# Optimization experiments

Hardware: AMD Instinct MI355X
Metric: run time of the kernel (lower is better)

The kernel has to match this reference:

```python
import jax, jax.numpy as jnp
import numpy as np

WS = 14          # window size (SAM ViT default)
NUM_HEADS = 12   # dim=768 -> head_dim=64
THETA = 10000.0  # rope theta


def _axial_rope_cos_sin(head_dim, end_x, end_y):
    # compute_axial_cis: head_dim//4 freqs per axis; t_x = t % end_x, t_y = t // end_x
    n = head_dim // 4
    freqs = 1.0 / (THETA ** (np.arange(0, head_dim, 4)[:n].astype(np.float32) / head_dim))
    t = np.arange(end_x * end_y, dtype=np.float32)
    t_x = t % end_x
    t_y = np.floor(t / end_x)
    ang = np.concatenate([t_x[:, None] * freqs[None, :], t_y[:, None] * freqs[None, :]], axis=-1)
    return jnp.asarray(np.cos(ang)), jnp.asarray(np.sin(ang))  # (N, head_dim//2) each


def _apply_rope(x, cos, sin):
    # x: (B, N, D) viewed as complex pairs along last dim (torch.view_as_complex ordering)
    x2 = x.reshape(x.shape[:-1] + (-1, 2))
    xr, xi = x2[..., 0], x2[..., 1]
    out_r = xr * cos - xi * sin
    out_i = xr * sin + xi * cos
    return jnp.stack([out_r, out_i], axis=-1).reshape(x.shape)


def setup_inputs() -> dict:
    key = jax.random.key(0)
    ks = jax.random.split(key, 6)
    B, H, W, C = 8, 64, 64, 768
    hd = C // NUM_HEADS
    max_rel = 2 * WS - 1
    return {
        "x": jax.random.normal(ks[0], (B, H, W, C), dtype=jnp.float32),
        "qkv_w": jax.random.normal(ks[1], (3 * C, C), dtype=jnp.float32) * 0.02,
        "qkv_b": jnp.zeros((3 * C,), dtype=jnp.float32),
        "proj_w": jax.random.normal(ks[2], (C, C), dtype=jnp.float32) * 0.02,
        "proj_b": jnp.zeros((C,), dtype=jnp.float32),
        "rel_pos_h": jax.random.normal(ks[3], (max_rel, hd), dtype=jnp.float32) * 0.02,
        "rel_pos_w": jax.random.normal(ks[4], (max_rel, hd), dtype=jnp.float32) * 0.02,
    }


def reference(x, qkv_w, qkv_b, proj_w, proj_b, rel_pos_h, rel_pos_w):
    B, H, W, C = x.shape
    nH = NUM_HEADS
    hd = C // nH
    N = WS * WS

    # --- window_partition with padding ---
    pad_h = (-H) % WS
    pad_w = (-W) % WS
    xp = jnp.pad(x, ((0, 0), (0, pad_h), (0, pad_w), (0, 0)))
    Hp, Wp = H + pad_h, W + pad_w
    nwh, nww = Hp // WS, Wp // WS
    xw = xp.reshape(B, nwh, WS, nww, WS, C).transpose(0, 1, 3, 2, 4, 5).reshape(-1, N, C)
    Bw = xw.shape[0]  # B * num_windows

    # --- qkv projection, split heads ---
    qkv = xw @ qkv_w.T + qkv_b                       # (Bw, N, 3C)
    qkv = qkv.reshape(Bw, N, 3, nH, hd).transpose(2, 0, 3, 1, 4).reshape(3, Bw * nH, N, hd)
    q, k, v = qkv[0], qkv[1], qkv[2]

    # --- 2D axial rotary encoding on q, k ---
    cos, sin = _axial_rope_cos_sin(hd, WS, WS)       # (N, hd//2)
    q = _apply_rope(q, cos, sin)
    k = _apply_rope(k, cos, sin)

    # --- decomposed relative-position bias (get_rel_pos gather + einsum) ---
    coords = jnp.arange(WS)[:, None] - jnp.arange(WS)[None, :] + (WS - 1)  # (WS, WS) in [0, 2WS-2]
    Rh = rel_pos_h[coords]                           # (WS, WS, hd)
    Rw = rel_pos_w[coords]
    r_q = q.reshape(-1, WS, WS, hd)
    rel_h = jnp.einsum('bhwc,hkc->bhwk', r_q, Rh)    # (BwnH, WS, WS, WS)
    rel_w = jnp.einsum('bhwc,wkc->bhwk', r_q, Rw)

    # --- attention: q k^T / sqrt(hd) + rel biases (math of concat_rel_pos + sdpa) ---
    attn = jnp.einsum('bqc,bkc->bqk', q, k) * (hd ** -0.5)
    attn = attn.reshape(-1, WS, WS, WS, WS) + rel_h[..., :, None] + rel_w[..., None, :]
    attn = jax.nn.softmax(attn.reshape(-1, N, N), axis=-1)
    out = attn @ v                                   # (BwnH, N, hd)

    # --- merge heads, output projection ---
    out = out.reshape(Bw, nH, WS, WS, hd).transpose(0, 2, 3, 1, 4).reshape(Bw, N, C)
    out = out @ proj_w.T + proj_b

    # --- window_unpartition, crop padding ---
    out = out.reshape(B, nwh, nww, WS, WS, C).transpose(0, 1, 3, 2, 4, 5).reshape(B, Hp, Wp, C)
    return out[:, :H, :W, :]
```

## Files before the change

### kernel.cpp

```cpp
#include <hip/hip_runtime.h>

using u16 = unsigned short;
using u32 = unsigned int;

typedef __bf16 bf16x8 __attribute__((ext_vector_type(8)));
typedef float f32x4 __attribute__((ext_vector_type(4)));

#define M32 32768

__device__ __forceinline__ u16 f2bf(float f) {
  u32 u = __float_as_uint(f);
  u += 0x7fffu + ((u >> 16) & 1u);
  return (u16)(u >> 16);
}
__device__ __forceinline__ u32 pkbf(float a, float b) {
  return (u32)f2bf(a) | ((u32)f2bf(b) << 16);
}
__device__ __forceinline__ u32 cvtpk(float a, float b) {
  u32 r; asm("v_cvt_pk_bf16_f32 %0, %1, %2" : "=v"(r) : "v"(a), "v"(b)); return r;
}
__device__ __forceinline__ float bflo(u32 w) { return __uint_as_float(w << 16); }
__device__ __forceinline__ float bfhi(u32 w) { return __uint_as_float(w & 0xffff0000u); }

__device__ __forceinline__ void async16(const void* g, void* l) {
  __builtin_amdgcn_global_load_lds((const __attribute__((address_space(1))) void*)g,
                                   (__attribute__((address_space(3))) void*)l, 16, 0, 0);
}

union frag { uint4 u; bf16x8 b; };

__global__ __launch_bounds__(256) void prep_w(const float* __restrict__ qw,
                                              const float* __restrict__ pw,
                                              u16* __restrict__ qwb, u16* __restrict__ pwb,
                                              float2* __restrict__ cs) {
  int i = blockIdx.x * 256 + threadIdx.x;
  if (i < 2304 * 768) qwb[i] = f2bf(qw[i]);
  if (i < 768 * 768)  pwb[i] = f2bf(pw[i]);
  if (i < 196 * 32) {
    int t = i >> 5, f = i & 31;
    float fr = powf(10000.f, -(float)(f & 15) * (1.f / 16.f));
    float ang = (f < 16 ? (float)(t % 14) : (float)(t / 14)) * fr;
    cs[i] = make_float2(cosf(ang), sinf(ang));
  }
}

template<int EPI>
__global__ __launch_bounds__(256) void gemm_bt(
    const void* __restrict__ Av, const u16* __restrict__ B,
    const float* __restrict__ bias, u16* __restrict__ Cb,
    float* __restrict__ Cf, int K, int N, int NTI)
{
  __shared__ u16 As[128 * 32];
  __shared__ u16 Bs[128 * 32];

  const int nwg = gridDim.x;
  const int orig = blockIdx.x;
  const int q = nwg >> 3, r = nwg & 7;
  const int xcd = orig & 7, loc = orig >> 3;
  const int wg = (xcd < r ? xcd * (q + 1) : r * (q + 1) + (xcd - r) * q) + loc;
  const int m0 = (wg / NTI) * 128;
  const int n0 = (wg % NTI) * 128;

  const int tid = threadIdx.x;
  const int lane = tid & 63;
  const int wv = tid >> 6;
  const int wm = wv >> 1, wn = wv & 1;
  const int lr = lane & 15, lq = lane >> 4;

  f32x4 acc[4][4];
#pragma unroll
  for (int i = 0; i < 4; i++)
#pragma unroll
    for (int j = 0; j < 4; j++)
      acc[i][j] = f32x4{0.f, 0.f, 0.f, 0.f};

  const int srow = tid >> 2, sg = (tid & 3) * 8;
  const float* Af0 = (const float*)Av + (size_t)(m0 + srow) * K + sg;
  const u16*   Ab0 = (const u16*)Av + (size_t)(m0 + srow) * K + sg;
  const u16*   B0  = B + (size_t)(n0 + srow) * K + sg;

  for (int k0 = 0; k0 < K; k0 += 32) {
    __syncthreads();
    async16(B0 + k0, (void*)(Bs + tid * 8));
    async16(B0 + (size_t)64 * K + k0, (void*)(Bs + 2048 + tid * 8));
    if constexpr (EPI == 0) {
      float4 a0 = *(const float4*)(Af0 + k0);
      float4 a1 = *(const float4*)(Af0 + k0 + 4);
      float4 a2 = *(const float4*)(Af0 + (size_t)64 * K + k0);
      float4 a3 = *(const float4*)(Af0 + (size_t)64 * K + k0 + 4);
      *(uint4*)(As + tid * 8) =
          make_uint4(cvtpk(a0.x, a0.y), cvtpk(a0.z, a0.w), cvtpk(a1.x, a1.y), cvtpk(a1.z, a1.w));
      *(uint4*)(As + 2048 + tid * 8) =
          make_uint4(cvtpk(a2.x, a2.y), cvtpk(a2.z, a2.w), cvtpk(a3.x, a3.y), cvtpk(a3.z, a3.w));
    } else {
      async16(Ab0 + k0, (void*)(As + tid * 8));
      async16(Ab0 + (size_t)64 * K + k0, (void*)(As + 2048 + tid * 8));
    }
    __syncthreads();

    frag af[4], bg[4];
#pragma unroll
    for (int i = 0; i < 4; i++) {
      af[i].u = *(const uint4*)(As + (wm * 64 + i * 16 + lr) * 32 + lq * 8);
      bg[i].u = *(const uint4*)(Bs + (wn * 64 + i * 16 + lr) * 32 + lq * 8);
    }
#pragma unroll
    for (int i = 0; i < 4; i++)
#pragma unroll
      for (int j = 0; j < 4; j++)
        acc[i][j] = __builtin_amdgcn_mfma_f32_16x16x32_bf16(af[i].b, bg[j].b, acc[i][j], 0, 0, 0);
  }

#pragma unroll
  for (int i = 0; i < 4; i++) {
#pragma unroll
    for (int j = 0; j < 4; j++) {
      const int n = n0 + wn * 64 + j * 16 + lr;
      const int mb = m0 + wm * 64 + i * 16 + lq * 4;
      const float bv = bias[n];
#pragma unroll
      for (int rr = 0; rr < 4; rr++) {
        float val = acc[i][j][rr] + bv;
        int m = mb + rr;
        if (EPI == 0) Cb[(size_t)m * N + n] = f2bf(val);
        else          Cf[(size_t)m * N + n] = val;
      }
    }
  }
}

#define R1P 104
#define VTP 232
#define PQP 40
#define LDS_R1   (224 * R1P * 2)
#define LDS_VT   (64 * VTP * 2)
#define LDS_PB   (4 * 16 * PQP * 2)
#define LDS_TOT  (LDS_R1 + LDS_VT + LDS_PB)

__global__ __launch_bounds__(256, 2) void attn_mfma(
    const u16* __restrict__ qkv, u16* __restrict__ ao,
    const float* __restrict__ relph, const float* __restrict__ relpw,
    const float2* __restrict__ cs, const float* __restrict__ qb)
{
  extern __shared__ char smem[];
  u16*   R1  = (u16*)smem;
  u16*   VTb = (u16*)(smem + LDS_R1);
  u16*   Th  = VTb;
  u16*   Tw  = VTb + 256 * 28;
  char*  PBr = smem + LDS_R1 + LDS_VT;

  const int blk = blockIdx.x;
  const int w = blk / 12, h = blk % 12;
  const int tid = threadIdx.x;
  const int lane = tid & 63, wv = tid >> 6;
  const int lr = lane & 15, lq = lane >> 4;

  const int b0 = w / 25, rw_ = w % 25;
  const int wy = (rw_ / 5) * 14, wx = (rw_ % 5) * 14;
  const int ty = tid / 14, tx = tid - ty * 14;
  const int gh = wy + ty, gw = wx + tx;
  const bool inb = (tid < 196) && (gh < 64) && (gw < 64);
  const size_t grow = (size_t)((b0 * 64 + gh) * 64 + gw);

  {
    float qf[64];
    if (tid < 196) {
      if (inb) {
        const u16* qp = qkv + grow * 2304 + h * 64;
        uint4 q4[8];
#pragma unroll
        for (int u = 0; u < 8; u++) q4[u] = *(const uint4*)(qp + u * 8);
#pragma unroll
        for (int u = 0; u < 8; u++) {
          qf[u*8+0] = bflo(q4[u].x); qf[u*8+1] = bfhi(q4[u].x);
          qf[u*8+2] = bflo(q4[u].y); qf[u*8+3] = bfhi(q4[u].y);
          qf[u*8+4] = bflo(q4[u].z); qf[u*8+5] = bfhi(q4[u].z);
          qf[u*8+6] = bflo(q4[u].w); qf[u*8+7] = bfhi(q4[u].w);
        }
      } else {
        const float4* bp = (const float4*)(qb + h * 64);
#pragma unroll
        for (int u = 0; u < 16; u++) {
          float4 t4 = bp[u];
          qf[u*4+0] = t4.x; qf[u*4+1] = t4.y; qf[u*4+2] = t4.z; qf[u*4+3] = t4.w;
        }
      }
      const float2* ct = cs + tid * 32;
#pragma unroll
      for (int f = 0; f < 32; f++) {
        float2 c2 = ct[f];
        float xr = qf[2*f], xi = qf[2*f+1];
        qf[2*f]   = (xr * c2.x - xi * c2.y) * 0.125f;
        qf[2*f+1] = (xr * c2.y + xi * c2.x) * 0.125f;
      }
    } else {
#pragma unroll
      for (int d = 0; d < 64; d++) qf[d] = 0.f;
    }
    if (tid < 224) {
      u16* dst = R1 + tid * R1P;
#pragma unroll
      for (int u = 0; u < 8; u++)
        *(uint4*)(dst + u * 8) = make_uint4(pkbf(qf[u*8+0], qf[u*8+1]), pkbf(qf[u*8+2], qf[u*8+3]),
                                            pkbf(qf[u*8+4], qf[u*8+5]), pkbf(qf[u*8+6], qf[u*8+7]));
    }
  }
  __syncthreads();

  frag af[4][3];
#pragma unroll
  for (int i = 0; i < 4; i++)
#pragma unroll
    for (int kc = 0; kc < 2; kc++) {
      if (wv == 3 && i >= 2)
        af[i][kc].u = make_uint4(0u, 0u, 0u, 0u);
      else
        af[i][kc].u = *(const uint4*)(R1 + (wv * 64 + i * 16 + lr) * R1P + kc * 32 + lq * 8);
    }

#pragma unroll
  for (int n = 0; n < 2; n++) {
    f32x4 tah[4], taw[4];
#pragma unroll
    for (int i = 0; i < 4; i++) { tah[i] = f32x4{0,0,0,0}; taw[i] = f32x4{0,0,0,0}; }
    const int j = n * 16 + lr;
#pragma unroll
    for (int kc = 0; kc < 2; kc++) {
      float4 ha = {0,0,0,0}, hb = {0,0,0,0}, wa = {0,0,0,0}, wb2 = {0,0,0,0};
      if (j < 27) {
        const float* ph  = relph + j * 64 + kc * 32 + lq * 8;
        const float* pw2 = relpw + j * 64 + kc * 32 + lq * 8;
        ha = *(const float4*)ph;  hb  = *(const float4*)(ph + 4);
        wa = *(const float4*)pw2; wb2 = *(const float4*)(pw2 + 4);
      }
      frag bh, bw;
      bh.u = make_uint4(pkbf(ha.x, ha.y), pkbf(ha.z, ha.w), pkbf(hb.x, hb.y), pkbf(hb.z, hb.w));
      bw.u = make_uint4(pkbf(wa.x, wa.y), pkbf(wa.z, wa.w), pkbf(wb2.x, wb2.y), pkbf(wb2.z, wb2.w));
#pragma unroll
      for (int i = 0; i < 4; i++) {
        tah[i] = __builtin_amdgcn_mfma_f32_16x16x32_bf16(af[i][kc].b, bh.b, tah[i], 0, 0, 0);
        taw[i] = __builtin_amdgcn_mfma_f32_16x16x32_bf16(af[i][kc].b, bw.b, taw[i], 0, 0, 0);
      }
    }
    int jcol = n * 16 + lr;
    if (jcol < 28) {
#pragma unroll
      for (int i = 0; i < 4; i++)
#pragma unroll
        for (int r2 = 0; r2 < 4; r2++) {
          int qq = wv * 64 + i * 16 + lq * 4 + r2;
          Th[qq * 28 + jcol] = f2bf(tah[i][r2] * 8.f);
          Tw[qq * 28 + jcol] = f2bf(taw[i][r2] * 8.f);
        }
    }
  }
  __syncthreads();

  {
    u32 wb[16];
#pragma unroll
    for (int z = 0; z < 16; z++) wb[z] = 0;
    if (tid < 196) {
      const u16* thr = Th + tid * 28 + ty + 13;
      const u16* twr = Tw + tid * 28 + tx + 13;
#pragma unroll
      for (int p = 0; p < 7; p++) wb[p]     = (u32)thr[-(2*p)] | ((u32)thr[-(2*p+1)] << 16);
#pragma unroll
      for (int p = 0; p < 7; p++) wb[7 + p] = (u32)twr[-(2*p)] | ((u32)twr[-(2*p+1)] << 16);
    }
    wb[14] = 0xC1F0u;
    if (tid < 224) {
      u16* dst = R1 + tid * R1P + 64;
#pragma unroll
      for (int u = 0; u < 4; u++)
        *(uint4*)(dst + u * 8) = make_uint4(wb[u*4], wb[u*4+1], wb[u*4+2], wb[u*4+3]);
    }
  }
  __syncthreads();

#pragma unroll
  for (int i = 0; i < 4; i++) {
    if (wv == 3 && i >= 2)
      af[i][2].u = make_uint4(0u, 0u, 0u, 0u);
    else
      af[i][2].u = *(const uint4*)(R1 + (wv * 64 + i * 16 + lr) * R1P + 64 + lq * 8);
  }
  __syncthreads();

  if (tid < 224) {
    const bool real = tid < 196;
    u32 kw[32];
#pragma unroll
    for (int z = 0; z < 32; z++) kw[z] = 0;
    if (real) {
      float kf[64];
      if (inb) {
        const u16* kp = qkv + grow * 2304 + 768 + h * 64;
        uint4 k4[8];
#pragma unroll
        for (int u = 0; u < 8; u++) k4[u] = *(const uint4*)(kp + u * 8);
#pragma unroll
        for (int u = 0; u < 8; u++) {
          kf[u*8+0] = bflo(k4[u].x); kf[u*8+1] = bfhi(k4[u].x);
          kf[u*8+2] = bflo(k4[u].y); kf[u*8+3] = bfhi(k4[u].y);
          kf[u*8+4] = bflo(k4[u].z); kf[u*8+5] = bfhi(k4[u].z);
          kf[u*8+6] = bflo(k4[u].w); kf[u*8+7] = bfhi(k4[u].w);
        }
      } else {
        const float4* bp = (const float4*)(qb + 768 + h * 64);
#pragma unroll
        for (int u = 0; u < 16; u++) {
          float4 t4 = bp[u];
          kf[u*4+0] = t4.x; kf[u*4+1] = t4.y; kf[u*4+2] = t4.z; kf[u*4+3] = t4.w;
        }
      }
      const float2* ct = cs + tid * 32;
#pragma unroll
      for (int f = 0; f < 32; f++) {
        float2 c2 = ct[f];
        float xr = kf[2*f], xi = kf[2*f+1];
        kf[2*f]   = xr * c2.x - xi * c2.y;
        kf[2*f+1] = xr * c2.y + xi * c2.x;
      }
#pragma unroll
      for (int p = 0; p < 32; p++) kw[p] = pkbf(kf[2*p], kf[2*p+1]);
    }
    const int tA = real ? 64 + ty : 92;
    const int tB = real ? 78 + tx : 92;
    u32 aw[16];
#pragma unroll
    for (int p = 0; p < 16; p++) {
      const int c0 = 64 + 2 * p, c1 = c0 + 1;
      u32 lo = (c0 == tA || c0 == tB) ? 0x3F80u : 0u;
      u32 hi = (c1 == tA || c1 == tB) ? 0x3F80u : 0u;
      aw[p] = lo | (hi << 16);
    }
    u16* dst = R1 + tid * R1P;
#pragma unroll
    for (int u = 0; u < 8; u++)
      *(uint4*)(dst + u * 8) = make_uint4(kw[u*4], kw[u*4+1], kw[u*4+2], kw[u*4+3]);
#pragma unroll
    for (int u = 0; u < 4; u++)
      *(uint4*)(dst + 64 + u * 8) = make_uint4(aw[u*4], aw[u*4+1], aw[u*4+2], aw[u*4+3]);

    if (real) {
      u16* col = VTb + tid;
      if (inb) {
        const u16* vp = qkv + grow * 2304 + 1536 + h * 64;
#pragma unroll
        for (int u = 0; u < 8; u++) {
          uint4 v4 = *(const uint4*)(vp + u * 8);
          col[(u*8+0) * VTP] = (u16)(v4.x & 0xffff); col[(u*8+1) * VTP] = (u16)(v4.x >> 16);
          col[(u*8+2) * VTP] = (u16)(v4.y & 0xffff); col[(u*8+3) * VTP] = (u16)(v4.y >> 16);
          col[(u*8+4) * VTP] = (u16)(v4.z & 0xffff); col[(u*8+5) * VTP] = (u16)(v4.z >> 16);
          col[(u*8+6) * VTP] = (u16)(v4.w & 0xffff); col[(u*8+7) * VTP] = (u16)(v4.w >> 16);
        }
      } else {
        const float4* bp = (const float4*)(qb + 1536 + h * 64);
#pragma unroll
        for (int u = 0; u < 16; u++) {
          float4 t4 = bp[u];
          col[(u*4+0) * VTP] = f2bf(t4.x); col[(u*4+1) * VTP] = f2bf(t4.y);
          col[(u*4+2) * VTP] = f2bf(t4.z); col[(u*4+3) * VTP] = f2bf(t4.w);
        }
      }
    } else {
#pragma unroll
      for (int d = 0; d < 64; d++) VTb[d * VTP + tid] = 0;
    }
  }
  __syncthreads();

  f32x4 oacc[4][4];
  f32x4 lacc[4];
#pragma unroll
  for (int i = 0; i < 4; i++) {
    lacc[i] = f32x4{0,0,0,0};
#pragma unroll
    for (int j = 0; j < 4; j++) oacc[i][j] = f32x4{0,0,0,0};
  }
  frag ones;
  ones.u = make_uint4(0x3F803F80u, 0x3F803F80u, 0x3F803F80u, 0x3F803F80u);
  u16* PB = (u16*)PBr + wv * 16 * PQP;

  for (int c = 0; c < 7; c++) {
    frag bk[2][3];
#pragma unroll
    for (int kt = 0; kt < 2; kt++)
#pragma unroll
      for (int kc = 0; kc < 3; kc++)
        bk[kt][kc].u = *(const uint4*)(R1 + (c * 32 + kt * 16 + lr) * R1P + kc * 32 + lq * 8);

    frag bv[4];
#pragma unroll
    for (int j = 0; j < 4; j++)
      bv[j].u = *(const uint4*)(VTb + (j * 16 + lr) * VTP + c * 32 + lq * 8);

    f32x4 sacc[4][2];
#pragma unroll
    for (int i = 0; i < 4; i++) { sacc[i][0] = f32x4{0,0,0,0}; sacc[i][1] = f32x4{0,0,0,0}; }
#pragma unroll
    for (int kc = 0; kc < 3; kc++)
#pragma unroll
      for (int i = 0; i < 4; i++)
#pragma unroll
        for (int kt = 0; kt < 2; kt++)
          sacc[i][kt] = __builtin_amdgcn_mfma_f32_16x16x32_bf16(af[i][kc].b, bk[kt][kc].b, sacc[i][kt], 0, 0, 0);

#pragma unroll
    for (int i = 0; i < 4; i++) {
#pragma unroll
      for (int kt = 0; kt < 2; kt++)
#pragma unroll
        for (int r2 = 0; r2 < 4; r2++)
          PB[(lq * 4 + r2) * PQP + kt * 16 + lr] = f2bf(__expf(sacc[i][kt][r2]));

      frag pf;
      pf.u = *(const uint4*)(PB + lr * PQP + lq * 8);

      lacc[i] = __builtin_amdgcn_mfma_f32_16x16x32_bf16(pf.b, ones.b, lacc[i], 0, 0, 0);
#pragma unroll
      for (int j = 0; j < 4; j++)
        oacc[i][j] = __builtin_amdgcn_mfma_f32_16x16x32_bf16(pf.b, bv[j].b, oacc[i][j], 0, 0, 0);
    }
  }

#pragma unroll
  for (int i = 0; i < 4; i++) {
    f32x4 inv;
#pragma unroll
    for (int r2 = 0; r2 < 4; r2++) inv[r2] = 1.f / lacc[i][r2];
#pragma unroll
    for (int r2 = 0; r2 < 4; r2++) {
      int qq = wv * 64 + i * 16 + lq * 4 + r2;
      if (qq < 196) {
        int qy = qq / 14, qx = qq - qy * 14;
        int gh2 = wy + qy, gw2 = wx + qx;
        if (gh2 < 64 && gw2 < 64) {
          u16* op = ao + (size_t)((b0 * 64 + gh2) * 64 + gw2) * 768 + h * 64 + lr;
#pragma unroll
          for (int j = 0; j < 4; j++)
            op[j * 16] = f2bf(oacc[i][j][r2] * inv[r2]);
        }
      }
    }
  }
}

extern "C" void kernel_launch(void* const* d_in, const int* in_sizes, int n_in,
                              void* d_out, int out_size, void* d_ws, size_t ws_size,
                              hipStream_t stream) {
  const float* x      = (const float*)d_in[0];
  const float* qkv_w  = (const float*)d_in[1];
  const float* qkv_b  = (const float*)d_in[2];
  const float* proj_w = (const float*)d_in[3];
  const float* proj_b = (const float*)d_in[4];
  const float* rel_h  = (const float*)d_in[5];
  const float* rel_w  = (const float*)d_in[6];
  float* out = (float*)d_out;

  char* ws = (char*)d_ws;
  u16* qkvb = (u16*)ws;
  u16* ao   = (u16*)(ws + (size_t)M32 * 2304 * 2);
  u16* qwb  = (u16*)(ws + (size_t)M32 * 2304 * 2 + (size_t)M32 * 768 * 2);
  u16* pwb  = qwb + 2304 * 768;
  float2* cs = (float2*)(pwb + 768 * 768);

  prep_w<<<6912, 256, 0, stream>>>(qkv_w, proj_w, qwb, pwb, cs);
  gemm_bt<0><<<dim3(256 * 18), 256, 0, stream>>>(x, qwb, qkv_b, qkvb, nullptr, 768, 2304, 18);
  attn_mfma<<<2400, 256, LDS_TOT, stream>>>(qkvb, ao, rel_h, rel_w, cs, qkv_b);
  gemm_bt<1><<<dim3(256 * 6), 256, 0, stream>>>(ao, pwb, proj_b, nullptr, out, 768, 768, 6);
}
```

Baseline: 556.1 us.

## Double-buffer GEMM shared-memory tiles to overlap global loads with MFMA

The bf16 GEMM kernel gets two shared-memory buffers for the A and B tiles. Each iteration now issues the next k-slice's async and global loads before the fragment reads and MFMAs on the current slice, leaving one barrier per iteration instead of two. The aim is to hide global-memory latency behind compute. In exchange the kernel doubles LDS use and keeps the prefetched fp32 A registers live across the MFMA block, which may lower occupancy.

```diff
diff --git a/kernel.cpp b/kernel.cpp
--- a/kernel.cpp
+++ b/kernel.cpp
@@ -50,8 +50,8 @@
     const float* __restrict__ bias, u16* __restrict__ Cb,
     float* __restrict__ Cf, int K, int N, int NTI)
 {
-  __shared__ u16 As[128 * 32];
-  __shared__ u16 Bs[128 * 32];
+  __shared__ u16 As[2][128 * 32];
+  __shared__ u16 Bs[2][128 * 32];
 
   const int nwg = gridDim.x;
   const int orig = blockIdx.x;
@@ -67,48 +67,81 @@
   const int wm = wv >> 1, wn = wv & 1;
   const int lr = lane & 15, lq = lane >> 4;
 
-  f32x4 acc[4][4];
-#pragma unroll
-  for (int i = 0; i < 4; i++)
-#pragma unroll
-    for (int j = 0; j < 4; j++)
-      acc[i][j] = f32x4{0.f, 0.f, 0.f, 0.f};
-
   const int srow = tid >> 2, sg = (tid & 3) * 8;
   const float* Af0 = (const float*)Av + (size_t)(m0 + srow) * K + sg;
   const u16*   Ab0 = (const u16*)Av + (size_t)(m0 + srow) * K + sg;
   const u16*   B0  = B + (size_t)(n0 + srow) * K + sg;
 
-  for (int k0 = 0; k0 < K; k0 += 32) {
-    __syncthreads();
-    async16(B0 + k0, (void*)(Bs + tid * 8));
-    async16(B0 + (size_t)64 * K + k0, (void*)(Bs + 2048 + tid * 8));
-    if constexpr (EPI == 0) {
-      float4 a0 = *(const float4*)(Af0 + k0);
-      float4 a1 = *(const float4*)(Af0 + k0 + 4);
-      float4 a2 = *(const float4*)(Af0 + (size_t)64 * K + k0);
-      float4 a3 = *(const float4*)(Af0 + (size_t)64 * K + k0 + 4);
-      *(uint4*)(As + tid * 8) =
+  async16(B0, (void*)(Bs[0] + tid * 8));
+  async16(B0 + (size_t)64 * K, (void*)(Bs[0] + 2048 + tid * 8));
+  if constexpr (EPI == 0) {
+    float4 a0 = *(const float4*)(Af0);
+    float4 a1 = *(const float4*)(Af0 + 4);
+    float4 a2 = *(const float4*)(Af0 + (size_t)64 * K);
+    float4 a3 = *(const float4*)(Af0 + (size_t)64 * K + 4);
+    *(uint4*)(As[0] + tid * 8) =
+        make_uint4(cvtpk(a0.x, a0.y), cvtpk(a0.z, a0.w), cvtpk(a1.x, a1.y), cvtpk(a1.z, a1.w));
+    *(uint4*)(As[0] + 2048 + tid * 8) =
+        make_uint4(cvtpk(a2.x, a2.y), cvtpk(a2.z, a2.w), cvtpk(a3.x, a3.y), cvtpk(a3.z, a3.w));
+  } else {
+    async16(Ab0, (void*)(As[0] + tid * 8));
+    async16(Ab0 + (size_t)64 * K, (void*)(As[0] + 2048 + tid * 8));
+  }
+  __syncthreads();
+
+  f32x4 acc[4][4];
+#pragma unroll
+  for (int i = 0; i < 4; i++)
+#pragma unroll
+    for (int j = 0; j < 4; j++)
+      acc[i][j] = f32x4{0.f, 0.f, 0.f, 0.f};
+
+  const int NT = K / 32;
+  for (int t = 0; t < NT; ++t) {
+    const int cur = t & 1;
+    const u16* Asc = As[cur];
+    const u16* Bsc = Bs[cur];
+    u16* Asn = As[cur ^ 1];
+    u16* Bsn = Bs[cur ^ 1];
+    const bool pre = (t + 1) < NT;
+    const int k1 = (t + 1) * 32;
+
+    float4 a0, a1, a2, a3;
+    if (pre) {
+      async16(B0 + k1, (void*)(Bsn + tid * 8));
+      async16(B0 + (size_t)64 * K + k1, (void*)(Bsn + 2048 + tid * 8));
+      if constexpr (EPI == 0) {
+        a0 = *(const float4*)(Af0 + k1);
+        a1 = *(const float4*)(Af0 + k1 + 4);
+        a2 = *(const float4*)(Af0 + (size_t)64 * K + k1);
+        a3 = *(const float4*)(Af0 + (size_t)64 * K + k1 + 4);
+      } else {
+        async16(Ab0 + k1, (void*)(Asn + tid * 8));
+        async16(Ab0 + (size_t)64 * K + k1, (void*)(Asn + 2048 + tid * 8));
+      }
+    }
+
+    frag af[4], bg[4];
+#pragma unroll
+    for (int i = 0; i < 4; i++) {
+      af[i].u = *(const uint4*)(Asc + (wm * 64 + i * 16 + lr) * 32 + lq * 8);
+      bg[i].u = *(const uint4*)(Bsc + (wn * 64 + i * 16 + lr) * 32 + lq * 8);
+    }
+
+    if (pre && EPI == 0) {
+      *(uint4*)(Asn + tid * 8) =
           make_uint4(cvtpk(a0.x, a0.y), cvtpk(a0.z, a0.w), cvtpk(a1.x, a1.y), cvtpk(a1.z, a1.w));
-      *(uint4*)(As + 2048 + tid * 8) =
+      *(uint4*)(Asn + 2048 + tid * 8) =
           make_uint4(cvtpk(a2.x, a2.y), cvtpk(a2.z, a2.w), cvtpk(a3.x, a3.y), cvtpk(a3.z, a3.w));
-    } else {
-      async16(Ab0 + k0, (void*)(As + tid * 8));
-      async16(Ab0 + (size_t)64 * K + k0, (void*)(As + 2048 + tid * 8));
-    }
-    __syncthreads();
-
-    frag af[4], bg[4];
-#pragma unroll
-    for (int i = 0; i < 4; i++) {
-      af[i].u = *(const uint4*)(As + (wm * 64 + i * 16 + lr) * 32 + lq * 8);
-      bg[i].u = *(const uint4*)(Bs + (wn * 64 + i * 16 + lr) * 32 + lq * 8);
-    }
+    }
+
 #pragma unroll
     for (int i = 0; i < 4; i++)
 #pragma unroll
       for (int j = 0; j < 4; j++)
         acc[i][j] = __builtin_amdgcn_mfma_f32_16x16x32_bf16(af[i].b, bg[j].b, acc[i][j], 0, 0, 0);
+
+    __syncthreads();
   }
 
 #pragma unroll
```

Measured after the change: 540.8 us. 1.03x faster.

## Double-buffer LDS and register-prefetch A tiles in GEMM main loop

Applied to the files above, without the earlier changes.

The bf16 GEMM kernel switches from a single shared-memory buffer with two barriers per k-step to double-buffered As/Bs tiles. The A operand is prefetched two iterations ahead into registers and B one iteration ahead via async loads. Explicit s_waitcnt counts and a single barrier per step let global loads overlap with the MFMA work. The cost is double the LDS use and more registers, which may lower occupancy, and hand-tuned vmcnt values that depend on how many loads are in flight.

```diff
diff --git a/kernel.cpp b/kernel.cpp
--- a/kernel.cpp
+++ b/kernel.cpp
@@ -44,14 +44,16 @@
   }
 }
 
+struct AR { float4 f[4]; uint4 u[2]; };
+
 template<int EPI>
 __global__ __launch_bounds__(256) void gemm_bt(
     const void* __restrict__ Av, const u16* __restrict__ B,
     const float* __restrict__ bias, u16* __restrict__ Cb,
     float* __restrict__ Cf, int K, int N, int NTI)
 {
-  __shared__ u16 As[128 * 32];
-  __shared__ u16 Bs[128 * 32];
+  __shared__ u16 As[2][128 * 32];
+  __shared__ u16 Bs[2][128 * 32];
 
   const int nwg = gridDim.x;
   const int orig = blockIdx.x;
@@ -67,49 +69,93 @@
   const int wm = wv >> 1, wn = wv & 1;
   const int lr = lane & 15, lq = lane >> 4;
 
-  f32x4 acc[4][4];
-#pragma unroll
-  for (int i = 0; i < 4; i++)
-#pragma unroll
-    for (int j = 0; j < 4; j++)
-      acc[i][j] = f32x4{0.f, 0.f, 0.f, 0.f};
-
   const int srow = tid >> 2, sg = (tid & 3) * 8;
   const float* Af0 = (const float*)Av + (size_t)(m0 + srow) * K + sg;
   const u16*   Ab0 = (const u16*)Av + (size_t)(m0 + srow) * K + sg;
   const u16*   B0  = B + (size_t)(n0 + srow) * K + sg;
 
-  for (int k0 = 0; k0 < K; k0 += 32) {
-    __syncthreads();
-    async16(B0 + k0, (void*)(Bs + tid * 8));
-    async16(B0 + (size_t)64 * K + k0, (void*)(Bs + 2048 + tid * 8));
-    if constexpr (EPI == 0) {
-      float4 a0 = *(const float4*)(Af0 + k0);
-      float4 a1 = *(const float4*)(Af0 + k0 + 4);
-      float4 a2 = *(const float4*)(Af0 + (size_t)64 * K + k0);
-      float4 a3 = *(const float4*)(Af0 + (size_t)64 * K + k0 + 4);
-      *(uint4*)(As + tid * 8) =
-          make_uint4(cvtpk(a0.x, a0.y), cvtpk(a0.z, a0.w), cvtpk(a1.x, a1.y), cvtpk(a1.z, a1.w));
-      *(uint4*)(As + 2048 + tid * 8) =
-          make_uint4(cvtpk(a2.x, a2.y), cvtpk(a2.z, a2.w), cvtpk(a3.x, a3.y), cvtpk(a3.z, a3.w));
-    } else {
-      async16(Ab0 + k0, (void*)(As + tid * 8));
-      async16(Ab0 + (size_t)64 * K + k0, (void*)(As + 2048 + tid * 8));
-    }
-    __syncthreads();
-
-    frag af[4], bg[4];
-#pragma unroll
-    for (int i = 0; i < 4; i++) {
-      af[i].u = *(const uint4*)(As + (wm * 64 + i * 16 + lr) * 32 + lq * 8);
-      bg[i].u = *(const uint4*)(Bs + (wn * 64 + i * 16 + lr) * 32 + lq * 8);
-    }
-#pragma unroll
-    for (int i = 0; i < 4; i++)
-#pragma unroll
-      for (int j = 0; j < 4; j++)
-        acc[i][j] = __builtin_amdgcn_mfma_f32_16x16x32_bf16(af[i].b, bg[j].b, acc[i][j], 0, 0, 0);
-  }
+#define LOADA(S, kk) { \
+    if constexpr (EPI == 0) { \
+      S.f[0] = *(const float4*)(Af0 + (kk)); \
+      S.f[1] = *(const float4*)(Af0 + (kk) + 4); \
+      S.f[2] = *(const float4*)(Af0 + (size_t)64 * K + (kk)); \
+      S.f[3] = *(const float4*)(Af0 + (size_t)64 * K + (kk) + 4); \
+    } else { \
+      S.u[0] = *(const uint4*)(Ab0 + (kk)); \
+      S.u[1] = *(const uint4*)(Ab0 + (size_t)64 * K + (kk)); \
+    } }
+
+#define WRITEA(S, buf) { \
+    if constexpr (EPI == 0) { \
+      *(uint4*)((buf) + tid * 8) = make_uint4( \
+          cvtpk(S.f[0].x, S.f[0].y), cvtpk(S.f[0].z, S.f[0].w), \
+          cvtpk(S.f[1].x, S.f[1].y), cvtpk(S.f[1].z, S.f[1].w)); \
+      *(uint4*)((buf) + 2048 + tid * 8) = make_uint4( \
+          cvtpk(S.f[2].x, S.f[2].y), cvtpk(S.f[2].z, S.f[2].w), \
+          cvtpk(S.f[3].x, S.f[3].y), cvtpk(S.f[3].z, S.f[3].w)); \
+    } else { \
+      *(uint4*)((buf) + tid * 8) = S.u[0]; \
+      *(uint4*)((buf) + 2048 + tid * 8) = S.u[1]; \
+    } }
+
+  AR s0, s1;
+  const int NT = K / 32;
+
+  LOADA(s0, 0);
+  LOADA(s1, 32);
+  async16(B0, (void*)(Bs[0] + tid * 8));
+  async16(B0 + (size_t)64 * K, (void*)(Bs[0] + 2048 + tid * 8));
+  WRITEA(s0, As[0]);
+  asm volatile("s_waitcnt vmcnt(0) lgkmcnt(0)" ::: "memory");
+  __builtin_amdgcn_s_barrier();
+
+  f32x4 acc[4][4];
+#pragma unroll
+  for (int i = 0; i < 4; i++)
+#pragma unroll
+    for (int j = 0; j < 4; j++)
+      acc[i][j] = f32x4{0.f, 0.f, 0.f, 0.f};
+
+#define GITER(t, SW, SL) { \
+    const int par = (t) & 1; \
+    const u16* Asc = As[par]; const u16* Bsc = Bs[par]; \
+    u16* Asn = As[par ^ 1];  u16* Bsn = Bs[par ^ 1]; \
+    const bool wrA = (t) + 1 < NT; \
+    const bool ldA = (t) + 2 < NT; \
+    if (wrA) { \
+      const int k1 = ((t) + 1) * 32; \
+      async16(B0 + k1, (void*)(Bsn + tid * 8)); \
+      async16(B0 + (size_t)64 * K + k1, (void*)(Bsn + 2048 + tid * 8)); \
+    } \
+    if (ldA) { LOADA(SL, ((t) + 2) * 32); } \
+    frag af[4], bg[4]; \
+    _Pragma("unroll") \
+    for (int i = 0; i < 4; i++) { \
+      af[i].u = *(const uint4*)(Asc + (wm * 64 + i * 16 + lr) * 32 + lq * 8); \
+      bg[i].u = *(const uint4*)(Bsc + (wn * 64 + i * 16 + lr) * 32 + lq * 8); \
+    } \
+    if (wrA) { WRITEA(SW, Asn); } \
+    _Pragma("unroll") \
+    for (int i = 0; i < 4; i++) \
+      _Pragma("unroll") \
+      for (int j = 0; j < 4; j++) \
+        acc[i][j] = __builtin_amdgcn_mfma_f32_16x16x32_bf16(af[i].b, bg[j].b, acc[i][j], 0, 0, 0); \
+    if (ldA) { \
+      if constexpr (EPI == 0) { asm volatile("s_waitcnt vmcnt(4) lgkmcnt(0)" ::: "memory"); } \
+      else                    { asm volatile("s_waitcnt vmcnt(2) lgkmcnt(0)" ::: "memory"); } \
+    } else { \
+      asm volatile("s_waitcnt vmcnt(0) lgkmcnt(0)" ::: "memory"); \
+    } \
+    __builtin_amdgcn_s_barrier(); \
+  }
+
+  for (int t = 0; t < NT; t += 2) {
+    GITER(t, s1, s0);
+    GITER(t + 1, s0, s1);
+  }
+#undef GITER
+#undef LOADA
+#undef WRITEA
 
 #pragma unroll
   for (int i = 0; i < 4; i++) {
```

Measured after the change: 612.8 us. +10.2%, slower.
